# Optimization experiments

Hardware: AMD Instinct MI355X
Metric: run time of the kernel (lower is better)

The kernel has to match this reference:

```python
import jax, jax.numpy as jnp
import numpy as np

NUMERICAL_STABILIZER = 1e-3


def relu_kernel(data, projection_matrix):
    # data: [B,L,H,D], projection_matrix: [M,D] -> [B,L,H,M]
    ratio = 1.0 / jnp.sqrt(jnp.asarray(projection_matrix.shape[0], dtype=data.dtype))
    data_dash = ratio * jnp.einsum('blhd,md->blhm', data, projection_matrix)
    return jax.nn.relu(data_dash) + NUMERICAL_STABILIZER


def favor_causal(query, key, value, projection_matrix):
    # query/key/value: [B,L,H,D]; projection_matrix: [M,D]
    qp = relu_kernel(query, projection_matrix)  # [B,L,H,M]
    kp = relu_kernel(key, projection_matrix)    # [B,L,H,M]
    # move L to scan axis: [L,B,H,*]
    qs = jnp.transpose(qp, (1, 0, 2, 3))
    ks = jnp.transpose(kp, (1, 0, 2, 3))
    vs = jnp.transpose(value, (1, 0, 2, 3))

    B, H, M = qs.shape[1], qs.shape[2], qs.shape[3]
    D = vs.shape[3]
    kv0 = jnp.zeros((B, H, M, D), dtype=qs.dtype)
    ksum0 = jnp.zeros((B, H, M), dtype=qs.dtype)

    def step(carry, inp):
        kv_sum, k_sum = carry
        q_t, k_t, v_t = inp  # [B,H,M], [B,H,M], [B,H,D]
        kv_sum = kv_sum + jnp.einsum('bhm,bhd->bhmd', k_t, v_t)
        k_sum = k_sum + k_t
        num_t = jnp.einsum('bhmd,bhm->bhd', kv_sum, q_t)  # [B,H,D]
        den_t = jnp.einsum('bhm,bhm->bh', q_t, k_sum)     # [B,H]
        return (kv_sum, k_sum), (num_t, den_t)

    _, (num, den) = jax.lax.scan(step, (kv0, ksum0), (qs, ks, vs))
    # num: [L,B,H,D], den: [L,B,H]
    out = num / den[..., None]
    return jnp.transpose(out, (1, 0, 2, 3))  # [B,L,H,D]


def setup_inputs() -> dict:
    key = jax.random.key(0)
    k1, k2, k3, k4 = jax.random.split(key, 4)
    B, L, H, D, M = 2, 4096, 8, 64, 128
    return {
        'query': jax.random.normal(k1, (B, L, H, D), dtype=jnp.float32),
        'key': jax.random.normal(k2, (B, L, H, D), dtype=jnp.float32),
        'value': jax.random.normal(k3, (B, L, H, D), dtype=jnp.float32),
        'projection_matrix': jax.random.normal(k4, (M, D), dtype=jnp.float32),
    }


def reference(query, key, value, projection_matrix):
    return favor_causal(query, key, value, projection_matrix)
```

## Files before the change

### kernel.cpp

```cpp
#include <hip/hip_runtime.h>


#define B_ 2
#define L_ 4096
#define H_ 8
#define D_ 64
#define M_ 128
#define BH_ 16
#define HD_ 512
#define LHD_ (L_*HD_)
#define C_ 64
#define T_ 64
#define RATIO 0.08838834764831845f
#define EPS 1e-3f
#define REC_CS 8320

#define VT_S 72
#define KF_S 136
#define SCR_SZ 9216

typedef __attribute__((ext_vector_type(8))) short bf16x8;
typedef __attribute__((ext_vector_type(4))) float f32x4;

__device__ __forceinline__ short f2bf(float f) {
  union { float f; unsigned u; } x; x.f = f;
  unsigned r = (x.u + 0x7fffu + ((x.u >> 16) & 1u)) >> 16;
  return (short)r;
}
__device__ __forceinline__ float bf2f(short s) {
  union { unsigned u; float f; } x; x.u = ((unsigned)(unsigned short)s) << 16;
  return x.f;
}
__device__ __forceinline__ bf16x8 load_cvt8(const float* p) {
  float4 a = *(const float4*)p;
  float4 b = *(const float4*)(p + 4);
  union { bf16x8 v; short s[8]; } u;
  u.s[0]=f2bf(a.x); u.s[1]=f2bf(a.y); u.s[2]=f2bf(a.z); u.s[3]=f2bf(a.w);
  u.s[4]=f2bf(b.x); u.s[5]=f2bf(b.y); u.s[6]=f2bf(b.z); u.s[7]=f2bf(b.w);
  return u.v;
}
#define MFMA(a,b,c) __builtin_amdgcn_mfma_f32_16x16x32_bf16((a),(b),(c),0,0,0)

__device__ __forceinline__ void stageVt(short* Vt, const float* __restrict__ vv,
                                        size_t gbase, int t0, int tid) {
  for (int fi = tid; fi < 64*16; fi += 256) {
    int t = fi >> 4, d4 = (fi & 15)*4;
    float4 v4 = *(const float4*)(vv + gbase + (size_t)(t0+t)*HD_ + d4);
    Vt[(d4+0)*VT_S + t] = f2bf(v4.x);
    Vt[(d4+1)*VT_S + t] = f2bf(v4.y);
    Vt[(d4+2)*VT_S + t] = f2bf(v4.z);
    Vt[(d4+3)*VT_S + t] = f2bf(v4.w);
  }
}

__device__ __forceinline__ void chunkSums(const short* Kft, const short* Vt,
    unsigned short* __restrict__ csb, int tid, int w, int quad, int l15)
{
  if (tid < 128) {
    float s = 0.f;
    #pragma unroll 8
    for (int t = 0; t < 64; ++t) s += bf2f(Kft[tid*VT_S + t]);
    csb[8192 + tid] = (unsigned short)f2bf(s);
  }
  bf16x8 av0 = *(const bf16x8*)&Vt[(16*w + l15)*VT_S + quad*8];
  bf16x8 av1 = *(const bf16x8*)&Vt[(16*w + l15)*VT_S + 32 + quad*8];
  #pragma unroll
  for (int mt = 0; mt < 8; ++mt) {
    f32x4 acc = {0.f,0.f,0.f,0.f};
    bf16x8 b0 = *(const bf16x8*)&Kft[(16*mt + l15)*VT_S + quad*8];
    bf16x8 b1 = *(const bf16x8*)&Kft[(16*mt + l15)*VT_S + 32 + quad*8];
    acc = MFMA(av0, b0, acc);
    acc = MFMA(av1, b1, acc);
    #pragma unroll
    for (int reg = 0; reg < 4; ++reg)
      csb[(16*w + 4*quad + reg)*128 + 16*mt + l15] = (unsigned short)f2bf(acc[reg]);
  }
}

__global__ __launch_bounds__(256, 2) void pA(
    const float* __restrict__ kk, const float* __restrict__ vv,
    const float* __restrict__ P, unsigned short* __restrict__ ws)
{
  __shared__ alignas(16) short Vt[64*VT_S];
  __shared__ alignas(16) short Scr[SCR_SZ];

  const int tid = threadIdx.x, w = tid >> 6, quad = (tid >> 4) & 3, l15 = tid & 15;
  const int cid = blockIdx.x, bh = cid >> 6, c = cid & 63;
  const size_t gbase = (size_t)(bh >> 3)*LHD_ + (size_t)(bh & 7)*D_;
  const int t0 = c*T_;
  unsigned short* csb = ws + (size_t)cid*REC_CS;

  stageVt(Vt, vv, gbase, t0, tid);

  const float* krow = kk + gbase + (size_t)(t0 + 16*w + l15)*HD_;
  bf16x8 ak0 = load_cvt8(krow + quad*8);
  bf16x8 ak1 = load_cvt8(krow + 32 + quad*8);
  #pragma unroll
  for (int ct = 0; ct < 8; ++ct) {
    const float* prow = P + (ct*16 + l15)*64;
    bf16x8 bp0 = load_cvt8(prow + quad*8);
    bf16x8 bp1 = load_cvt8(prow + 32 + quad*8);
    f32x4 ka = {0.f,0.f,0.f,0.f};
    ka = MFMA(ak0,bp0,ka); ka = MFMA(ak1,bp1,ka);
    #pragma unroll
    for (int reg = 0; reg < 4; ++reg)
      Scr[(16*ct + l15)*VT_S + 16*w + 4*quad + reg] =
          f2bf(fmaxf(ka[reg]*RATIO, 0.f) + EPS);
  }
  __syncthreads();
  chunkSums(Scr, Vt, csb, tid, w, quad, l15);
}

__global__ __launch_bounds__(256) void pB(unsigned short* __restrict__ ws) {
  const int gid = blockIdx.x*256 + threadIdx.x;
  if (gid >= BH_*(REC_CS/2)) return;
  const int bh = gid / (REC_CS/2), rem = gid % (REC_CS/2);
  unsigned short* base = ws + (size_t)bh*C_*REC_CS + (size_t)rem*2;
  float r0 = 0.f, r1 = 0.f;
  for (int c = 0; c < C_; c += 4) {
    unsigned u[4];
    #pragma unroll
    for (int j = 0; j < 4; ++j)
      u[j] = *(const unsigned*)(base + (size_t)(c+j)*REC_CS);
    #pragma unroll
    for (int j = 0; j < 4; ++j) {
      unsigned pw = (unsigned)(unsigned short)f2bf(r0)
                  | ((unsigned)(unsigned short)f2bf(r1) << 16);
      *(unsigned*)(base + (size_t)(c+j)*REC_CS) = pw;
      r0 += bf2f((short)(u[j] & 0xffffu));
      r1 += bf2f((short)(u[j] >> 16));
    }
  }
}

__global__ __launch_bounds__(256, 2) void pC(
    const float* __restrict__ qq, const float* __restrict__ kk,
    const float* __restrict__ vv, const float* __restrict__ P,
    const unsigned short* __restrict__ ws, float* __restrict__ out)
{
  __shared__ alignas(16) short Vt[64*VT_S];
  __shared__ alignas(16) short Kf1[64*KF_S];
  __shared__ alignas(16) short Scr[SCR_SZ];
  __shared__ float ksl[128];

  const int tid = threadIdx.x, w = tid >> 6, quad = (tid >> 4) & 3, l15 = tid & 15;
  const int cid = blockIdx.x, bh = cid >> 6, c = cid & 63;
  const size_t gbase = (size_t)(bh >> 3)*LHD_ + (size_t)(bh & 7)*D_;
  const int t0 = c*T_;
  const unsigned short* csb = ws + (size_t)cid*REC_CS;

  stageVt(Vt, vv, gbase, t0, tid);

  const float* qrow = qq + gbase + (size_t)(t0 + 16*w + l15)*HD_;
  const float* krow = kk + gbase + (size_t)(t0 + 16*w + l15)*HD_;
  bf16x8 aq0 = load_cvt8(qrow + quad*8);
  bf16x8 aq1 = load_cvt8(qrow + 32 + quad*8);
  bf16x8 ak0 = load_cvt8(krow + quad*8);
  bf16x8 ak1 = load_cvt8(krow + 32 + quad*8);
  #pragma unroll
  for (int ct = 0; ct < 8; ++ct) {
    const float* prow = P + (ct*16 + l15)*64;
    bf16x8 bp0 = load_cvt8(prow + quad*8);
    bf16x8 bp1 = load_cvt8(prow + 32 + quad*8);
    f32x4 qa = {0.f,0.f,0.f,0.f}, ka = {0.f,0.f,0.f,0.f};
    qa = MFMA(aq0,bp0,qa); qa = MFMA(aq1,bp1,qa);
    ka = MFMA(ak0,bp0,ka); ka = MFMA(ak1,bp1,ka);
    #pragma unroll
    for (int reg = 0; reg < 4; ++reg) {
      int trow = 16*w + 4*quad + reg;
      int m = 16*ct + l15;
      Scr[trow*KF_S + m] = f2bf(fmaxf(qa[reg]*RATIO, 0.f) + EPS);
      Kf1[trow*KF_S + m] = f2bf(fmaxf(ka[reg]*RATIO, 0.f) + EPS);
    }
  }
  bf16x8 qfr[4];
  #pragma unroll
  for (int k2 = 0; k2 < 4; ++k2)
    qfr[k2] = *(const bf16x8*)&Scr[(16*w + l15)*KF_S + k2*32 + quad*8];
  if (tid < 128) ksl[tid] = bf2f((short)csb[8192 + tid]);
  __syncthreads();

  f32x4 nacc[4];
  #pragma unroll
  for (int ct = 0; ct < 4; ++ct) { f32x4 z = {0.f,0.f,0.f,0.f}; nacc[ct] = z; }
  #pragma unroll
  for (int k2 = 0; k2 < 4; ++k2)
    #pragma unroll
    for (int ct = 0; ct < 4; ++ct) {
      bf16x8 bb = *(const bf16x8*)(csb + (16*ct + l15)*128 + k2*32 + quad*8);
      nacc[ct] = MFMA(qfr[k2], bb, nacc[ct]);
    }

  float dp = 0.f;
  #pragma unroll
  for (int k2 = 0; k2 < 4; ++k2)
    #pragma unroll
    for (int j = 0; j < 8; ++j)
      dp += bf2f(qfr[k2][j]) * ksl[k2*32 + quad*8 + j];
  dp += __shfl_xor(dp, 16);
  dp += __shfl_xor(dp, 32);

  f32x4 sacc[4];
  #pragma unroll
  for (int jt = 0; jt < 4; ++jt) { f32x4 z = {0.f,0.f,0.f,0.f}; sacc[jt] = z; }
  #pragma unroll
  for (int k2 = 0; k2 < 4; ++k2)
    #pragma unroll
    for (int jt = 0; jt < 4; ++jt) {
      bf16x8 bb = *(const bf16x8*)&Kf1[(16*jt + l15)*KF_S + k2*32 + quad*8];
      sacc[jt] = MFMA(qfr[k2], bb, sacc[jt]);
    }
  float rs[4] = {0.f,0.f,0.f,0.f};
  #pragma unroll
  for (int jt = 0; jt < 4; ++jt)
    #pragma unroll
    for (int reg = 0; reg < 4; ++reg) {
      int row = 16*w + 4*quad + reg;
      int j = 16*jt + l15;
      float val = (j <= row) ? sacc[jt][reg] : 0.f;
      rs[reg] += val;
      Scr[row*VT_S + j] = f2bf(val);
    }
  #pragma unroll
  for (int reg = 0; reg < 4; ++reg) {
    rs[reg] += __shfl_xor(rs[reg], 1);
    rs[reg] += __shfl_xor(rs[reg], 2);
    rs[reg] += __shfl_xor(rs[reg], 4);
    rs[reg] += __shfl_xor(rs[reg], 8);
  }

  #pragma unroll
  for (int kx = 0; kx < 2; ++kx) {
    bf16x8 a = *(const bf16x8*)&Scr[(16*w + l15)*VT_S + kx*32 + quad*8];
    #pragma unroll
    for (int ct = 0; ct < 4; ++ct) {
      bf16x8 bb = *(const bf16x8*)&Vt[(16*ct + l15)*VT_S + kx*32 + quad*8];
      nacc[ct] = MFMA(a, bb, nacc[ct]);
    }
  }

  #pragma unroll
  for (int reg = 0; reg < 4; ++reg) {
    float den1 = __shfl(dp, 4*quad + reg);
    float inv = 1.f / (den1 + rs[reg]);
    int trow = t0 + 16*w + 4*quad + reg;
    #pragma unroll
    for (int ct = 0; ct < 4; ++ct)
      out[gbase + (size_t)trow*HD_ + 16*ct + l15] = nacc[ct][reg] * inv;
  }
}

extern "C" void kernel_launch(void* const* d_in, const int* in_sizes, int n_in,
                              void* d_out, int out_size, void* d_ws, size_t ws_size,
                              hipStream_t stream) {
  const float* q = (const float*)d_in[0];
  const float* k = (const float*)d_in[1];
  const float* v = (const float*)d_in[2];
  const float* P = (const float*)d_in[3];
  float* out = (float*)d_out;
  unsigned short* ws = (unsigned short*)d_ws;

  pA<<<dim3(BH_*C_), dim3(256), 0, stream>>>(k, v, P, ws);
  pB<<<dim3((BH_*(REC_CS/2) + 255)/256), dim3(256), 0, stream>>>(ws);
  pC<<<dim3(BH_*C_), dim3(256), 0, stream>>>(q, k, v, P, ws, out);
}
```

Baseline: 153.3 us.

## Compute Q/K features once in first pass and stash bf16 tiles in workspace

The first kernel now projects both query and key, writes bf16 feature maps and transposed V to workspace, and computes key column sums via shuffles instead of a serial loop. The final kernel then reads these precomputed bf16 tiles instead of reloading fp32 q/k/v and redoing the projection, and uses less shared memory for higher occupancy. The prefix-scan kernel gains register double-buffering of loads. This trades recomputation for extra workspace traffic.

```diff
diff --git a/kernel.cpp b/kernel.cpp
--- a/kernel.cpp
+++ b/kernel.cpp
@@ -13,11 +13,15 @@
 #define T_ 64
 #define RATIO 0.08838834764831845f
 #define EPS 1e-3f
+
 #define REC_CS 8320
+#define REC_F  8192
+#define REC_V  4096
+#define QF_OFF ((size_t)BH_*C_*REC_CS)
+#define KF_OFF (QF_OFF + (size_t)BH_*C_*REC_F)
+#define VT_OFF (KF_OFF + (size_t)BH_*C_*REC_F)
 
 #define VT_S 72
-#define KF_S 136
-#define SCR_SZ 9216
 
 typedef __attribute__((ext_vector_type(8))) short bf16x8;
 typedef __attribute__((ext_vector_type(4))) float f32x4;
@@ -41,8 +45,24 @@
 }
 #define MFMA(a,b,c) __builtin_amdgcn_mfma_f32_16x16x32_bf16((a),(b),(c),0,0,0)
 
-__device__ __forceinline__ void stageVt(short* Vt, const float* __restrict__ vv,
-                                        size_t gbase, int t0, int tid) {
+__global__ __launch_bounds__(256, 2) void K1(
+    const float* __restrict__ qq, const float* __restrict__ kk,
+    const float* __restrict__ vv, const float* __restrict__ P,
+    unsigned short* __restrict__ ws)
+{
+  __shared__ alignas(16) short Vt[64*VT_S];
+  __shared__ alignas(16) short Kft[128*VT_S];
+  __shared__ float ksp[4][128];
+
+  const int tid = threadIdx.x, w = tid >> 6, quad = (tid >> 4) & 3, l15 = tid & 15;
+  const int cid = blockIdx.x, bh = cid >> 6, c = cid & 63;
+  const size_t gbase = (size_t)(bh >> 3)*LHD_ + (size_t)(bh & 7)*D_;
+  const int t0 = c*T_;
+  unsigned short* csb = ws + (size_t)cid*REC_CS;
+  unsigned short* qfb = ws + QF_OFF + (size_t)cid*REC_F;
+  unsigned short* kfb = ws + KF_OFF + (size_t)cid*REC_F;
+  unsigned short* vtb = ws + VT_OFF + (size_t)cid*REC_V;
+
   for (int fi = tid; fi < 64*16; fi += 256) {
     int t = fi >> 4, d4 = (fi & 15)*4;
     float4 v4 = *(const float4*)(vv + gbase + (size_t)(t0+t)*HD_ + d4);
@@ -51,105 +71,6 @@
     Vt[(d4+2)*VT_S + t] = f2bf(v4.z);
     Vt[(d4+3)*VT_S + t] = f2bf(v4.w);
   }
-}
-
-__device__ __forceinline__ void chunkSums(const short* Kft, const short* Vt,
-    unsigned short* __restrict__ csb, int tid, int w, int quad, int l15)
-{
-  if (tid < 128) {
-    float s = 0.f;
-    #pragma unroll 8
-    for (int t = 0; t < 64; ++t) s += bf2f(Kft[tid*VT_S + t]);
-    csb[8192 + tid] = (unsigned short)f2bf(s);
-  }
-  bf16x8 av0 = *(const bf16x8*)&Vt[(16*w + l15)*VT_S + quad*8];
-  bf16x8 av1 = *(const bf16x8*)&Vt[(16*w + l15)*VT_S + 32 + quad*8];
-  #pragma unroll
-  for (int mt = 0; mt < 8; ++mt) {
-    f32x4 acc = {0.f,0.f,0.f,0.f};
-    bf16x8 b0 = *(const bf16x8*)&Kft[(16*mt + l15)*VT_S + quad*8];
-    bf16x8 b1 = *(const bf16x8*)&Kft[(16*mt + l15)*VT_S + 32 + quad*8];
-    acc = MFMA(av0, b0, acc);
-    acc = MFMA(av1, b1, acc);
-    #pragma unroll
-    for (int reg = 0; reg < 4; ++reg)
-      csb[(16*w + 4*quad + reg)*128 + 16*mt + l15] = (unsigned short)f2bf(acc[reg]);
-  }
-}
-
-__global__ __launch_bounds__(256, 2) void pA(
-    const float* __restrict__ kk, const float* __restrict__ vv,
-    const float* __restrict__ P, unsigned short* __restrict__ ws)
-{
-  __shared__ alignas(16) short Vt[64*VT_S];
-  __shared__ alignas(16) short Scr[SCR_SZ];
-
-  const int tid = threadIdx.x, w = tid >> 6, quad = (tid >> 4) & 3, l15 = tid & 15;
-  const int cid = blockIdx.x, bh = cid >> 6, c = cid & 63;
-  const size_t gbase = (size_t)(bh >> 3)*LHD_ + (size_t)(bh & 7)*D_;
-  const int t0 = c*T_;
-  unsigned short* csb = ws + (size_t)cid*REC_CS;
-
-  stageVt(Vt, vv, gbase, t0, tid);
-
-  const float* krow = kk + gbase + (size_t)(t0 + 16*w + l15)*HD_;
-  bf16x8 ak0 = load_cvt8(krow + quad*8);
-  bf16x8 ak1 = load_cvt8(krow + 32 + quad*8);
-  #pragma unroll
-  for (int ct = 0; ct < 8; ++ct) {
-    const float* prow = P + (ct*16 + l15)*64;
-    bf16x8 bp0 = load_cvt8(prow + quad*8);
-    bf16x8 bp1 = load_cvt8(prow + 32 + quad*8);
-    f32x4 ka = {0.f,0.f,0.f,0.f};
-    ka = MFMA(ak0,bp0,ka); ka = MFMA(ak1,bp1,ka);
-    #pragma unroll
-    for (int reg = 0; reg < 4; ++reg)
-      Scr[(16*ct + l15)*VT_S + 16*w + 4*quad + reg] =
-          f2bf(fmaxf(ka[reg]*RATIO, 0.f) + EPS);
-  }
-  __syncthreads();
-  chunkSums(Scr, Vt, csb, tid, w, quad, l15);
-}
-
-__global__ __launch_bounds__(256) void pB(unsigned short* __restrict__ ws) {
-  const int gid = blockIdx.x*256 + threadIdx.x;
-  if (gid >= BH_*(REC_CS/2)) return;
-  const int bh = gid / (REC_CS/2), rem = gid % (REC_CS/2);
-  unsigned short* base = ws + (size_t)bh*C_*REC_CS + (size_t)rem*2;
-  float r0 = 0.f, r1 = 0.f;
-  for (int c = 0; c < C_; c += 4) {
-    unsigned u[4];
-    #pragma unroll
-    for (int j = 0; j < 4; ++j)
-      u[j] = *(const unsigned*)(base + (size_t)(c+j)*REC_CS);
-    #pragma unroll
-    for (int j = 0; j < 4; ++j) {
-      unsigned pw = (unsigned)(unsigned short)f2bf(r0)
-                  | ((unsigned)(unsigned short)f2bf(r1) << 16);
-      *(unsigned*)(base + (size_t)(c+j)*REC_CS) = pw;
-      r0 += bf2f((short)(u[j] & 0xffffu));
-      r1 += bf2f((short)(u[j] >> 16));
-    }
-  }
-}
-
-__global__ __launch_bounds__(256, 2) void pC(
-    const float* __restrict__ qq, const float* __restrict__ kk,
-    const float* __restrict__ vv, const float* __restrict__ P,
-    const unsigned short* __restrict__ ws, float* __restrict__ out)
-{
-  __shared__ alignas(16) short Vt[64*VT_S];
-  __shared__ alignas(16) short Kf1[64*KF_S];
-  __shared__ alignas(16) short Scr[SCR_SZ];
-  __shared__ float ksl[128];
-
-  const int tid = threadIdx.x, w = tid >> 6, quad = (tid >> 4) & 3, l15 = tid & 15;
-  const int cid = blockIdx.x, bh = cid >> 6, c = cid & 63;
-  const size_t gbase = (size_t)(bh >> 3)*LHD_ + (size_t)(bh & 7)*D_;
-  const int t0 = c*T_;
-  const unsigned short* csb = ws + (size_t)cid*REC_CS;
-
-  stageVt(Vt, vv, gbase, t0, tid);
 
   const float* qrow = qq + gbase + (size_t)(t0 + 16*w + l15)*HD_;
   const float* krow = kk + gbase + (size_t)(t0 + 16*w + l15)*HD_;
@@ -165,20 +86,108 @@
     f32x4 qa = {0.f,0.f,0.f,0.f}, ka = {0.f,0.f,0.f,0.f};
     qa = MFMA(aq0,bp0,qa); qa = MFMA(aq1,bp1,qa);
     ka = MFMA(ak0,bp0,ka); ka = MFMA(ak1,bp1,ka);
+    float s = 0.f;
     #pragma unroll
     for (int reg = 0; reg < 4; ++reg) {
       int trow = 16*w + 4*quad + reg;
       int m = 16*ct + l15;
-      Scr[trow*KF_S + m] = f2bf(fmaxf(qa[reg]*RATIO, 0.f) + EPS);
-      Kf1[trow*KF_S + m] = f2bf(fmaxf(ka[reg]*RATIO, 0.f) + EPS);
-    }
-  }
-  bf16x8 qfr[4];
+      float qv = fmaxf(qa[reg]*RATIO, 0.f) + EPS;
+      float kv = fmaxf(ka[reg]*RATIO, 0.f) + EPS;
+      short ks_ = f2bf(kv);
+      qfb[trow*128 + m] = (unsigned short)f2bf(qv);
+      kfb[trow*128 + m] = (unsigned short)ks_;
+      Kft[m*VT_S + trow] = ks_;
+      s += kv;
+    }
+    s += __shfl_xor(s, 16);
+    s += __shfl_xor(s, 32);
+    if (quad == 0) ksp[w][16*ct + l15] = s;
+  }
+  __syncthreads();
+
+  for (int fi = tid; fi < 64*8; fi += 256) {
+    int d = fi >> 3, part = fi & 7;
+    *(bf16x8*)(vtb + d*64 + part*8) = *(const bf16x8*)&Vt[d*VT_S + part*8];
+  }
+  if (tid < 128)
+    csb[8192 + tid] = (unsigned short)f2bf(
+        ksp[0][tid] + ksp[1][tid] + ksp[2][tid] + ksp[3][tid]);
+
+  bf16x8 av0 = *(const bf16x8*)&Vt[(16*w + l15)*VT_S + quad*8];
+  bf16x8 av1 = *(const bf16x8*)&Vt[(16*w + l15)*VT_S + 32 + quad*8];
+  #pragma unroll
+  for (int mt = 0; mt < 8; ++mt) {
+    f32x4 acc = {0.f,0.f,0.f,0.f};
+    bf16x8 b0 = *(const bf16x8*)&Kft[(16*mt + l15)*VT_S + quad*8];
+    bf16x8 b1 = *(const bf16x8*)&Kft[(16*mt + l15)*VT_S + 32 + quad*8];
+    acc = MFMA(av0, b0, acc);
+    acc = MFMA(av1, b1, acc);
+    #pragma unroll
+    for (int reg = 0; reg < 4; ++reg)
+      csb[(16*w + 4*quad + reg)*128 + 16*mt + l15] = (unsigned short)f2bf(acc[reg]);
+  }
+}
+
+__global__ __launch_bounds__(256) void K2(unsigned short* __restrict__ ws) {
+  const int gid = blockIdx.x*256 + threadIdx.x;
+  if (gid >= BH_*(REC_CS/2)) return;
+  const int bh = gid / (REC_CS/2), rem = gid % (REC_CS/2);
+  unsigned short* base = ws + (size_t)bh*C_*REC_CS + (size_t)rem*2;
+  float r0 = 0.f, r1 = 0.f;
+  unsigned cur[4], nxt[4];
+  #pragma unroll
+  for (int j = 0; j < 4; ++j)
+    cur[j] = *(const unsigned*)(base + (size_t)j*REC_CS);
+  for (int b = 0; b < 16; ++b) {
+    if (b < 15) {
+      #pragma unroll
+      for (int j = 0; j < 4; ++j)
+        nxt[j] = *(const unsigned*)(base + (size_t)(4*b+4+j)*REC_CS);
+    }
+    #pragma unroll
+    for (int j = 0; j < 4; ++j) {
+      unsigned pw = (unsigned)(unsigned short)f2bf(r0)
+                  | ((unsigned)(unsigned short)f2bf(r1) << 16);
+      *(unsigned*)(base + (size_t)(4*b+j)*REC_CS) = pw;
+      r0 += bf2f((short)(cur[j] & 0xffffu));
+      r1 += bf2f((short)(cur[j] >> 16));
+    }
+    if (b < 15) {
+      #pragma unroll
+      for (int j = 0; j < 4; ++j) cur[j] = nxt[j];
+    }
+  }
+}
+
+__global__ __launch_bounds__(256, 4) void K3(
+    const unsigned short* __restrict__ ws, float* __restrict__ out)
+{
+  __shared__ alignas(16) short Sm[64*VT_S];
+
+  const int tid = threadIdx.x, w = tid >> 6, quad = (tid >> 4) & 3, l15 = tid & 15;
+  const int cid = blockIdx.x, bh = cid >> 6, c = cid & 63;
+  const size_t gbase = (size_t)(bh >> 3)*LHD_ + (size_t)(bh & 7)*D_;
+  const int t0 = c*T_;
+  const unsigned short* csb = ws + (size_t)cid*REC_CS;
+  const unsigned short* qfb = ws + QF_OFF + (size_t)cid*REC_F;
+  const unsigned short* kfb = ws + KF_OFF + (size_t)cid*REC_F;
+  const unsigned short* vtb = ws + VT_OFF + (size_t)cid*REC_V;
+
+  bf16x8 qf[4];
   #pragma unroll
   for (int k2 = 0; k2 < 4; ++k2)
-    qfr[k2] = *(const bf16x8*)&Scr[(16*w + l15)*KF_S + k2*32 + quad*8];
-  if (tid < 128) ksl[tid] = bf2f((short)csb[8192 + tid]);
-  __syncthreads();
+    qf[k2] = *(const bf16x8*)(qfb + (16*w + l15)*128 + k2*32 + quad*8);
+
+  float dp = 0.f;
+  #pragma unroll
+  for (int k2 = 0; k2 < 4; ++k2) {
+    bf16x8 kv8 = *(const bf16x8*)(csb + 8192 + k2*32 + quad*8);
+    #pragma unroll
+    for (int j = 0; j < 8; ++j)
+      dp += bf2f(qf[k2][j]) * bf2f(kv8[j]);
+  }
+  dp += __shfl_xor(dp, 16);
+  dp += __shfl_xor(dp, 32);
 
   f32x4 nacc[4];
   #pragma unroll
@@ -188,27 +197,18 @@
     #pragma unroll
     for (int ct = 0; ct < 4; ++ct) {
       bf16x8 bb = *(const bf16x8*)(csb + (16*ct + l15)*128 + k2*32 + quad*8);
-      nacc[ct] = MFMA(qfr[k2], bb, nacc[ct]);
-    }
-
-  float dp = 0.f;
+      nacc[ct] = MFMA(qf[k2], bb, nacc[ct]);
+    }
+
+  f32x4 sacc[4];
+  #pragma unroll
+  for (int jt = 0; jt < 4; ++jt) { f32x4 z = {0.f,0.f,0.f,0.f}; sacc[jt] = z; }
   #pragma unroll
   for (int k2 = 0; k2 < 4; ++k2)
     #pragma unroll
-    for (int j = 0; j < 8; ++j)
-      dp += bf2f(qfr[k2][j]) * ksl[k2*32 + quad*8 + j];
-  dp += __shfl_xor(dp, 16);
-  dp += __shfl_xor(dp, 32);
-
-  f32x4 sacc[4];
-  #pragma unroll
-  for (int jt = 0; jt < 4; ++jt) { f32x4 z = {0.f,0.f,0.f,0.f}; sacc[jt] = z; }
-  #pragma unroll
-  for (int k2 = 0; k2 < 4; ++k2)
-    #pragma unroll
     for (int jt = 0; jt < 4; ++jt) {
-      bf16x8 bb = *(const bf16x8*)&Kf1[(16*jt + l15)*KF_S + k2*32 + quad*8];
-      sacc[jt] = MFMA(qfr[k2], bb, sacc[jt]);
+      bf16x8 bb = *(const bf16x8*)(kfb + (16*jt + l15)*128 + k2*32 + quad*8);
+      sacc[jt] = MFMA(qf[k2], bb, sacc[jt]);
     }
   float rs[4] = {0.f,0.f,0.f,0.f};
   #pragma unroll
@@ -219,7 +219,7 @@
       int j = 16*jt + l15;
       float val = (j <= row) ? sacc[jt][reg] : 0.f;
       rs[reg] += val;
-      Scr[row*VT_S + j] = f2bf(val);
+      Sm[row*VT_S + j] = f2bf(val);
     }
   #pragma unroll
   for (int reg = 0; reg < 4; ++reg) {
@@ -231,10 +231,10 @@
 
   #pragma unroll
   for (int kx = 0; kx < 2; ++kx) {
-    bf16x8 a = *(const bf16x8*)&Scr[(16*w + l15)*VT_S + kx*32 + quad*8];
+    bf16x8 a = *(const bf16x8*)&Sm[(16*w + l15)*VT_S + kx*32 + quad*8];
     #pragma unroll
     for (int ct = 0; ct < 4; ++ct) {
-      bf16x8 bb = *(const bf16x8*)&Vt[(16*ct + l15)*VT_S + kx*32 + quad*8];
+      bf16x8 bb = *(const bf16x8*)(vtb + (16*ct + l15)*64 + kx*32 + quad*8);
       nacc[ct] = MFMA(a, bb, nacc[ct]);
     }
   }
@@ -260,7 +260,7 @@
   float* out = (float*)d_out;
   unsigned short* ws = (unsigned short*)d_ws;
 
-  pA<<<dim3(BH_*C_), dim3(256), 0, stream>>>(k, v, P, ws);
-  pB<<<dim3((BH_*(REC_CS/2) + 255)/256), dim3(256), 0, stream>>>(ws);
-  pC<<<dim3(BH_*C_), dim3(256), 0, stream>>>(q, k, v, P, ws, out);
-}
+  K1<<<dim3(BH_*C_), dim3(256), 0, stream>>>(q, k, v, P, ws);
+  K2<<<dim3((BH_*(REC_CS/2) + 255)/256), dim3(256), 0, stream>>>(ws);
+  K3<<<dim3(BH_*C_), dim3(256), 0, stream>>>(ws, out);
+}
```

Measured after the change: 153.2 us. Within noise of the previous version (-0.1%).
